# Optimization experiments

Measured on AMD Instinct MI355X. Metric: run time of the kernel, lower is better.

Reference implementation:

```python
import jax, jax.numpy as jnp
import numpy as np

K = 1024          # number of knots (len(self.knots))
SAMPLES = 4096    # outSamples
S = SAMPLES - 1   # xIter has samples-1 points


def irregular_gauss(x, mean, low_std, high_std):
    # std = lowStd if x <= mean else highStd; std = exp(std)
    std = jnp.exp(jnp.where(x <= mean, low_std, high_std))
    return jnp.exp(-0.5 * jnp.square((x - mean) / std))


def setup_inputs() -> dict:
    key = jax.random.key(0)
    ks = jax.random.split(key, 8)
    x = jax.random.uniform(ks[0], (K,), dtype=jnp.float32)
    smear_window = jnp.array([0.125, 0.125], dtype=jnp.float32)  # (lowerSmear, upperSmear)
    knot_mean = 0.1 * jax.random.normal(ks[1], (K,), dtype=jnp.float32)
    knot_low = 0.1 * jax.random.normal(ks[2], (K,), dtype=jnp.float32)
    knot_high = 0.1 * jax.random.normal(ks[3], (K,), dtype=jnp.float32)
    ent_mean = 0.1 * jax.random.normal(ks[4], (K,), dtype=jnp.float32)
    ent_low = 0.1 * jax.random.normal(ks[5], (K,), dtype=jnp.float32)
    ent_high = 0.1 * jax.random.normal(ks[6], (K,), dtype=jnp.float32)
    polarization = 0.1 * jax.random.normal(ks[7], (K,), dtype=jnp.float32)
    return {"x": x, "smear_window": smear_window, "knot_mean": knot_mean,
            "knot_low": knot_low, "knot_high": knot_high, "ent_mean": ent_mean,
            "ent_low": ent_low, "ent_high": ent_high, "polarization": polarization}


def reference(x, smear_window, knot_mean, knot_low, knot_high,
              ent_mean, ent_low, ent_high, polarization):
    lower, upper = smear_window[0], smear_window[1]
    x_step = ((upper - lower) * x) / SAMPLES            # [K]
    x_low = (1.0 - lower) * x                           # [K]
    x_iter = jnp.arange(S, dtype=x.dtype) / SAMPLES     # [S]

    # per-knot smear curves: knot_k applied over its smeared window  -> [K, S]
    grid = x_step[:, None] * x_iter[None, :] + x_low[:, None]
    smear = irregular_gauss(grid, knot_mean[:, None], knot_low[:, None], knot_high[:, None])
    signal = jnp.fft.fft(smear, axis=-1)                # [K, S] complex

    # correlation_ij = mean_s ifft(sig_i * conj(sig_j))  ==  (sig_i[0]*conj(sig_j[0])) / S
    corr = (signal[:, None, 0] * jnp.conj(signal[None, :, 0])).real / S  # [K, K]
    # entangleActivation[j] (a LinearGuass) applied to correlation_ij
    mix = irregular_gauss(corr, ent_mean[None, :], ent_low[None, :], ent_high[None, :])
    mask = 1.0 - jnp.eye(K, dtype=x.dtype)              # skip idx == jdx
    mixm = mix * mask                                   # [K, K]

    # superposition = outer(sig_j, sig_i); row/col collapse then ifft.
    # By FFT linearity: ifft(sig_i * sum(sig_j)) = sum(sig_j) * smear_i, and symmetrically.
    sum_sig = jnp.sum(signal, axis=-1)                  # [K] complex; smears are real -> Re used
    cosp, sinp = jnp.cos(polarization), jnp.sin(polarization)

    coef1 = mixm @ (cosp * sum_sig.real)                                 # [K]
    term1 = coef1[:, None] * smear                                       # cos branch
    term2 = sum_sig.real[:, None] * jnp.einsum('ij,js->is', mixm * sinp[None, :], smear)  # sin branch
    term3 = jnp.sum(mask - mixm, axis=1)[:, None] * smear                # classical mix (1-mix)*smear
    result = jnp.sum(term1 + term2 + term3, axis=0)                      # [S]

    # trailing gaussian envelope, summed over knots
    lows = (1.0 - lower) * x
    highs = (1.0 + upper) * x
    g_samples = (highs - lows)[:, None] * x_iter[None, :] + lows[:, None]  # [K, S]
    gauss = irregular_gauss(g_samples, x[:, None], lows[:, None], highs[:, None])
    return jnp.sum(gauss, axis=0) * result              # [S]
```

## Files before the change

### kernel.cpp

```cpp
#include <hip/hip_runtime.h>
#include <math.h>

#define K 1024
#define SAMPLES 4096
#define S (SAMPLES - 1)

__device__ __forceinline__ float ig(float x, float mean, float lo, float hi) {
    float sel = (x <= mean) ? lo : hi;
    float z = (x - mean) * __expf(-sel);
    return __expf(-0.5f * z * z);
}

__device__ __forceinline__ float block_reduce256(float v, float* sm) {
    #pragma unroll
    for (int o = 32; o > 0; o >>= 1) v += __shfl_down(v, o, 64);
    int lane = threadIdx.x & 63, w = threadIdx.x >> 6;
    if (lane == 0) sm[w] = v;
    __syncthreads();
    float r = 0.f;
    if (threadIdx.x == 0) r = sm[0] + sm[1] + sm[2] + sm[3];
    __syncthreads();
    return r;
}

__global__ __launch_bounds__(256) void k_smear_sums(
    const float* __restrict__ x, const float* __restrict__ sw,
    const float* __restrict__ km, const float* __restrict__ kl, const float* __restrict__ kh,
    float* __restrict__ A, float* __restrict__ R)
{
    __shared__ float sm[4];
    int k = blockIdx.x;
    float lower = sw[0], upper = sw[1];
    float xk = x[k];
    float x_step = (upper - lower) * xk * (1.0f / SAMPLES);
    float x_low = (1.0f - lower) * xk;
    float mean = km[k], lo = kl[k], hi = kh[k];
    float sum = 0.f;
    for (int s = threadIdx.x; s < S; s += 256) {
        float g = x_step * ((float)s * (1.0f / SAMPLES)) + x_low;
        sum += ig(g, mean, lo, hi);
    }
    float tot = block_reduce256(sum, sm);
    if (threadIdx.x == 0) {
        A[k] = tot;
        R[k] = (float)S * ig(x_low, mean, lo, hi);
    }
}

__global__ __launch_bounds__(256) void k_weights(
    const float* __restrict__ A, const float* __restrict__ R,
    const float* __restrict__ em, const float* __restrict__ el, const float* __restrict__ eh,
    const float* __restrict__ pol, float* __restrict__ w)
{
    __shared__ float sm0[4], sm1[4], sm2[4];
    int t = blockIdx.x;
    float At = A[t];
    float emt = em[t], elt = el[t], eht = eh[t];
    float c = 0.f, m = 0.f, cs = 0.f;
    for (int u = threadIdx.x; u < K; u += 256) {
        if (u == t) continue;
        float corr = At * A[u] * (1.0f / S);
        float mr = ig(corr, em[u], el[u], eh[u]);
        float mc = ig(corr, emt, elt, eht);
        float Ru = R[u];
        c += mr * __cosf(pol[u]) * Ru;
        m += mr;
        cs += Ru * mc;
    }
    float ct = block_reduce256(c, sm0);
    float mt = block_reduce256(m, sm1);
    float cst = block_reduce256(cs, sm2);
    if (threadIdx.x == 0)
        w[t] = ct + __sinf(pol[t]) * cst + (float)(K - 1) - mt;
}

__global__ __launch_bounds__(256) void k_output(
    const float* __restrict__ x, const float* __restrict__ sw,
    const float* __restrict__ km, const float* __restrict__ kl, const float* __restrict__ kh,
    const float* __restrict__ w, float* __restrict__ out)
{
    int t = blockIdx.x * 256 + threadIdx.x;
    int s = t >> 4;
    int sub = t & 15;
    if (s >= S) return;
    float xi = (float)s * (1.0f / SAMPLES);
    float lower = sw[0], upper = sw[1];
    float rsum = 0.f, esum = 0.f;
    for (int k = sub; k < K; k += 16) {
        float xk = x[k];
        float x_step = (upper - lower) * xk * (1.0f / SAMPLES);
        float x_low = (1.0f - lower) * xk;
        float smear = ig(x_step * xi + x_low, km[k], kl[k], kh[k]);
        rsum += w[k] * smear;
        float highs = (1.0f + upper) * xk;
        float g = (highs - x_low) * xi + x_low;
        esum += ig(g, xk, x_low, highs);
    }
    #pragma unroll
    for (int o = 8; o > 0; o >>= 1) {
        rsum += __shfl_down(rsum, o, 16);
        esum += __shfl_down(esum, o, 16);
    }
    if (sub == 0) out[s] = rsum * esum;
}

extern "C" void kernel_launch(void* const* d_in, const int* in_sizes, int n_in,
                              void* d_out, int out_size, void* d_ws, size_t ws_size,
                              hipStream_t stream)
{
    const float* x   = (const float*)d_in[0];
    const float* sw  = (const float*)d_in[1];
    const float* km  = (const float*)d_in[2];
    const float* kl  = (const float*)d_in[3];
    const float* kh  = (const float*)d_in[4];
    const float* em  = (const float*)d_in[5];
    const float* el  = (const float*)d_in[6];
    const float* eh  = (const float*)d_in[7];
    const float* pol = (const float*)d_in[8];
    float* out = (float*)d_out;

    float* A = (float*)d_ws;
    float* R = A + K;
    float* w = R + K;

    k_smear_sums<<<K, 256, 0, stream>>>(x, sw, km, kl, kh, A, R);
    k_weights<<<K, 256, 0, stream>>>(A, R, em, el, eh, pol, w);
    k_output<<<(SAMPLES * 16) / 256, 256, 0, stream>>>(x, sw, km, kl, kh, w, out);
}
```

Measured before the change: 94.93 us.

## Fuse three kernels into one cooperative kernel with grid syncs

Merges the smear-sum, weight and output kernels into a single cooperative launch of 1024 blocks that separates the phases with grid.sync. This removes two kernel launch boundaries. It also precomputes cos(pol)*R per knot so the weights loop skips a cosine per pair. The output phase now gives each sample a full 64-lane wavefront instead of 16 lanes, which needs 1024 blocks to cover all samples, so the kernel relies on 1024 blocks being co-resident for the cooperative launch.

```diff
diff --git a/kernel.cpp b/kernel.cpp
--- a/kernel.cpp
+++ b/kernel.cpp
@@ -1,5 +1,8 @@
 #include <hip/hip_runtime.h>
+#include <hip/hip_cooperative_groups.h>
 #include <math.h>
+
+namespace cg = cooperative_groups;
 
 #define K 1024
 #define SAMPLES 4096
@@ -23,85 +26,88 @@
     return r;
 }
 
-__global__ __launch_bounds__(256) void k_smear_sums(
+__global__ __launch_bounds__(256, 4) void k_all(
     const float* __restrict__ x, const float* __restrict__ sw,
     const float* __restrict__ km, const float* __restrict__ kl, const float* __restrict__ kh,
-    float* __restrict__ A, float* __restrict__ R)
+    const float* __restrict__ em, const float* __restrict__ el, const float* __restrict__ eh,
+    const float* __restrict__ pol,
+    float* __restrict__ A, float* __restrict__ R, float* __restrict__ CR,
+    float* __restrict__ w, float* __restrict__ out)
 {
-    __shared__ float sm[4];
-    int k = blockIdx.x;
+    cg::grid_group grid = cg::this_grid();
+    __shared__ float sm0[4], sm1[4], sm2[4];
+
     float lower = sw[0], upper = sw[1];
-    float xk = x[k];
-    float x_step = (upper - lower) * xk * (1.0f / SAMPLES);
-    float x_low = (1.0f - lower) * xk;
-    float mean = km[k], lo = kl[k], hi = kh[k];
-    float sum = 0.f;
-    for (int s = threadIdx.x; s < S; s += 256) {
-        float g = x_step * ((float)s * (1.0f / SAMPLES)) + x_low;
-        sum += ig(g, mean, lo, hi);
-    }
-    float tot = block_reduce256(sum, sm);
-    if (threadIdx.x == 0) {
-        A[k] = tot;
-        R[k] = (float)S * ig(x_low, mean, lo, hi);
-    }
-}
 
-__global__ __launch_bounds__(256) void k_weights(
-    const float* __restrict__ A, const float* __restrict__ R,
-    const float* __restrict__ em, const float* __restrict__ el, const float* __restrict__ eh,
-    const float* __restrict__ pol, float* __restrict__ w)
-{
-    __shared__ float sm0[4], sm1[4], sm2[4];
-    int t = blockIdx.x;
-    float At = A[t];
-    float emt = em[t], elt = el[t], eht = eh[t];
-    float c = 0.f, m = 0.f, cs = 0.f;
-    for (int u = threadIdx.x; u < K; u += 256) {
-        if (u == t) continue;
-        float corr = At * A[u] * (1.0f / S);
-        float mr = ig(corr, em[u], el[u], eh[u]);
-        float mc = ig(corr, emt, elt, eht);
-        float Ru = R[u];
-        c += mr * __cosf(pol[u]) * Ru;
-        m += mr;
-        cs += Ru * mc;
-    }
-    float ct = block_reduce256(c, sm0);
-    float mt = block_reduce256(m, sm1);
-    float cst = block_reduce256(cs, sm2);
-    if (threadIdx.x == 0)
-        w[t] = ct + __sinf(pol[t]) * cst + (float)(K - 1) - mt;
-}
-
-__global__ __launch_bounds__(256) void k_output(
-    const float* __restrict__ x, const float* __restrict__ sw,
-    const float* __restrict__ km, const float* __restrict__ kl, const float* __restrict__ kh,
-    const float* __restrict__ w, float* __restrict__ out)
-{
-    int t = blockIdx.x * 256 + threadIdx.x;
-    int s = t >> 4;
-    int sub = t & 15;
-    if (s >= S) return;
-    float xi = (float)s * (1.0f / SAMPLES);
-    float lower = sw[0], upper = sw[1];
-    float rsum = 0.f, esum = 0.f;
-    for (int k = sub; k < K; k += 16) {
+    {
+        int k = blockIdx.x;
         float xk = x[k];
         float x_step = (upper - lower) * xk * (1.0f / SAMPLES);
         float x_low = (1.0f - lower) * xk;
-        float smear = ig(x_step * xi + x_low, km[k], kl[k], kh[k]);
-        rsum += w[k] * smear;
-        float highs = (1.0f + upper) * xk;
-        float g = (highs - x_low) * xi + x_low;
-        esum += ig(g, xk, x_low, highs);
+        float mean = km[k], lo = kl[k], hi = kh[k];
+        float sum = 0.f;
+        for (int s = threadIdx.x; s < S; s += 256) {
+            float g = x_step * ((float)s * (1.0f / SAMPLES)) + x_low;
+            sum += ig(g, mean, lo, hi);
+        }
+        float tot = block_reduce256(sum, sm0);
+        if (threadIdx.x == 0) {
+            A[k] = tot;
+            float Rk = (float)S * ig(x_low, mean, lo, hi);
+            R[k] = Rk;
+            CR[k] = __cosf(pol[k]) * Rk;
+        }
     }
-    #pragma unroll
-    for (int o = 8; o > 0; o >>= 1) {
-        rsum += __shfl_down(rsum, o, 16);
-        esum += __shfl_down(esum, o, 16);
+    grid.sync();
+
+    {
+        int t = blockIdx.x;
+        float At = A[t];
+        float emt = em[t], elt = el[t], eht = eh[t];
+        float c = 0.f, m = 0.f, cs = 0.f;
+        for (int u = threadIdx.x; u < K; u += 256) {
+            if (u == t) continue;
+            float corr = At * A[u] * (1.0f / S);
+            float mr = ig(corr, em[u], el[u], eh[u]);
+            float mc = ig(corr, emt, elt, eht);
+            c += mr * CR[u];
+            m += mr;
+            cs += R[u] * mc;
+        }
+        float ct = block_reduce256(c, sm0);
+        float mt = block_reduce256(m, sm1);
+        float cst = block_reduce256(cs, sm2);
+        if (threadIdx.x == 0)
+            w[t] = ct + __sinf(pol[t]) * cst + (float)(K - 1) - mt;
     }
-    if (sub == 0) out[s] = rsum * esum;
+    grid.sync();
+
+    {
+        int tid = blockIdx.x * 256 + threadIdx.x;
+        int s = tid >> 6;
+        int lane = tid & 63;
+        if (s < S) {
+            float xi = (float)s * (1.0f / SAMPLES);
+            float rsum = 0.f, esum = 0.f;
+            #pragma unroll 4
+            for (int k = lane; k < K; k += 64) {
+                float xk = x[k];
+                float x_step = (upper - lower) * xk * (1.0f / SAMPLES);
+                float x_low = (1.0f - lower) * xk;
+                float smear = ig(x_step * xi + x_low, km[k], kl[k], kh[k]);
+                rsum += w[k] * smear;
+                float highs = (1.0f + upper) * xk;
+                float g = (highs - x_low) * xi + x_low;
+                esum += ig(g, xk, x_low, highs);
+            }
+            #pragma unroll
+            for (int o = 32; o > 0; o >>= 1) {
+                rsum += __shfl_down(rsum, o, 64);
+                esum += __shfl_down(esum, o, 64);
+            }
+            if (lane == 0) out[s] = rsum * esum;
+        }
+    }
 }
 
 extern "C" void kernel_launch(void* const* d_in, const int* in_sizes, int n_in,
@@ -119,11 +125,13 @@
     const float* pol = (const float*)d_in[8];
     float* out = (float*)d_out;
 
-    float* A = (float*)d_ws;
-    float* R = A + K;
-    float* w = R + K;
+    float* A  = (float*)d_ws;
+    float* R  = A + K;
+    float* CR = R + K;
+    float* w  = CR + K;
 
-    k_smear_sums<<<K, 256, 0, stream>>>(x, sw, km, kl, kh, A, R);
-    k_weights<<<K, 256, 0, stream>>>(A, R, em, el, eh, pol, w);
-    k_output<<<(SAMPLES * 16) / 256, 256, 0, stream>>>(x, sw, km, kl, kh, w, out);
+    void* args[] = {(void*)&x, (void*)&sw, (void*)&km, (void*)&kl, (void*)&kh,
+                    (void*)&em, (void*)&el, (void*)&eh, (void*)&pol,
+                    (void*)&A, (void*)&R, (void*)&CR, (void*)&w, (void*)&out};
+    hipLaunchCooperativeKernel((void*)k_all, dim3(K), dim3(256), args, 0, stream);
 }
```

New measurement: 252.1 us. 2.66x slower.
